# Optimization experiments

Hardware: AMD Instinct MI355X
Metric: run time of the kernel (lower is better)

Reference implementation:

```python
import jax, jax.numpy as jnp
import numpy as np

N_HEAD, D_MODEL, D_HEAD = 16, 1024, 64
QLEN, BSZ, RLEN = 2048, 2, 2048
SCALE = 1.0 / (D_HEAD ** 0.5)


def _rel_shift(x):
    # x: (qlen, rlen, bsz, n_head) -- faithful port of the pad/reshape trick
    q, r, b, n = x.shape
    zero_pad = jnp.zeros((q, 1, b, n), dtype=x.dtype)
    x_padded = jnp.concatenate([zero_pad, x], axis=1)      # (q, r+1, b, n)
    x_padded = x_padded.reshape(r + 1, q, b, n)
    return x_padded[1:].reshape(q, r, b, n)


def setup_inputs() -> dict:
    key = jax.random.key(0)
    ks = jax.random.split(key, 8)
    w = jax.random.normal(ks[0], (QLEN, BSZ, D_MODEL), dtype=jnp.float32)
    r = jax.random.normal(ks[1], (RLEN, D_MODEL), dtype=jnp.float32)
    attn_mask = jax.random.randint(ks[2], (RLEN, BSZ), 0, 2).astype(bool)  # (klen, bsz) key padding
    s = 0.02
    qkv_w = jax.random.normal(ks[3], (D_MODEL, 3 * N_HEAD * D_HEAD), dtype=jnp.float32) * s
    r_net_w = jax.random.normal(ks[4], (D_MODEL, N_HEAD * D_HEAD), dtype=jnp.float32) * s
    o_w = jax.random.normal(ks[5], (N_HEAD * D_HEAD, D_MODEL), dtype=jnp.float32) * s
    r_w_bias = jax.random.normal(ks[6], (N_HEAD, D_HEAD), dtype=jnp.float32) * s
    r_r_bias = jax.random.normal(ks[7], (N_HEAD, D_HEAD), dtype=jnp.float32) * s
    return {"w": w, "r": r, "attn_mask": attn_mask, "qkv_w": qkv_w,
            "r_net_w": r_net_w, "o_w": o_w, "r_w_bias": r_w_bias, "r_r_bias": r_r_bias}


def reference(w, r, attn_mask, qkv_w, r_net_w, o_w, r_w_bias, r_r_bias):
    qlen, bsz, _ = w.shape
    rlen = r.shape[0]
    klen = qlen  # no mems
    heads = w @ qkv_w                                   # (q, b, 3*H)
    wq, wk, wv = jnp.split(heads, 3, axis=-1)
    wq = wq.reshape(qlen, bsz, N_HEAD, D_HEAD)
    wk = wk.reshape(klen, bsz, N_HEAD, D_HEAD)
    wv = wv.reshape(klen, bsz, N_HEAD, D_HEAD)
    r_head_k = (r @ r_net_w).reshape(rlen, N_HEAD, D_HEAD)
    # NOTE: original code sets r_w_bias = self.r_r_bias (bug preserved faithfully)
    rw_head_q = wq + r_r_bias[None, None]               # (q, b, n, d)
    rr_head_q = wq + r_r_bias[None, None]
    AC = jnp.einsum('qbnd,kbnd->bnqk', rw_head_q, wk)
    BD = jnp.einsum('qbnd,rnd->bnqr', rr_head_q, r_head_k)
    BD = jnp.transpose(BD, (2, 3, 0, 1))                # (q, r, b, n)
    BD = _rel_shift(BD)
    BD = jnp.transpose(BD, (2, 3, 0, 1))[:, :, :, :klen]  # (b, n, q, k)
    attn_score = (AC + BD) * SCALE
    # 2D mask broadcast semantics: (klen, bsz) key-padding mask
    attn_score = jnp.where(attn_mask.T[:, None, None, :], -jnp.inf, attn_score)
    attn_prob = jax.nn.softmax(attn_score.astype(jnp.float32), axis=-1)
    attn_prob = jnp.where(jnp.isnan(attn_prob), 0.0, attn_prob).astype(attn_score.dtype)
    coverage = attn_prob
    attn_vec = jnp.einsum('bnqk,kbnd->qbnd', attn_prob, wv)
    attn_vec = attn_vec.reshape(qlen, bsz, N_HEAD * D_HEAD)
    output = attn_vec @ o_w                             # (q, b, d_model)
    return (output, coverage)
```

## Files before the change

### kernel.cpp

```cpp
#include <hip/hip_runtime.h>
#include <hip/hip_bf16.h>


#define QL 2048
#define KL 2048
#define RL 2048
#define BS 2
#define NHD 16
#define DH 64
#define DM 1024

typedef __hip_bfloat16 bf16;
typedef short v8s __attribute__((ext_vector_type(8)));
typedef float v4f __attribute__((ext_vector_type(4)));

__device__ __forceinline__ bf16 f2b(float x) { return __float2bfloat16(x); }
__device__ __forceinline__ short f2s(float x) {
    return __builtin_bit_cast(short, __float2bfloat16(x));
}

template <int EPI>
__global__ __launch_bounds__(256) void gemm64f(
    const float* __restrict__ A, const float* __restrict__ B,
    int M, int N, int K,
    float* __restrict__ C,
    bf16* __restrict__ Qb, bf16* __restrict__ Wk, bf16* __restrict__ Wvt,
    bf16* __restrict__ Rk, const float* __restrict__ rrb)
{
    __shared__ short As[64][40];
    __shared__ short Bs[64][40];
    const int n0 = blockIdx.x * 64, m0 = blockIdx.y * 64;
    const int t = threadIdx.x, w = t >> 6, lane = t & 63;
    const int quad = lane >> 4, lr = lane & 15;

    v4f acc[4] = {};
    for (int k0 = 0; k0 < K; k0 += 32) {
        {
            const int row = t >> 2, cg = (t & 3) << 3;
            const float* ap = A + (size_t)(m0 + row) * K + k0 + cg;
            float4 a0 = *(const float4*)ap;
            float4 a1 = *(const float4*)(ap + 4);
            v8s pk;
            pk[0] = f2s(a0.x); pk[1] = f2s(a0.y); pk[2] = f2s(a0.z); pk[3] = f2s(a0.w);
            pk[4] = f2s(a1.x); pk[5] = f2s(a1.y); pk[6] = f2s(a1.z); pk[7] = f2s(a1.w);
            *(v8s*)&As[row][cg] = pk;
            const int kk = t >> 3, ng = (t & 7) << 3;
            const float* bp = B + (size_t)(k0 + kk) * N + n0 + ng;
            float4 b0 = *(const float4*)bp;
            float4 b1 = *(const float4*)(bp + 4);
            Bs[ng + 0][kk] = f2s(b0.x); Bs[ng + 1][kk] = f2s(b0.y);
            Bs[ng + 2][kk] = f2s(b0.z); Bs[ng + 3][kk] = f2s(b0.w);
            Bs[ng + 4][kk] = f2s(b1.x); Bs[ng + 5][kk] = f2s(b1.y);
            Bs[ng + 6][kk] = f2s(b1.z); Bs[ng + 7][kk] = f2s(b1.w);
        }
        __syncthreads();
        v8s af = *(const v8s*)&As[16 * w + lr][quad * 8];
#pragma unroll
        for (int ct = 0; ct < 4; ++ct) {
            v8s bfm = *(const v8s*)&Bs[ct * 16 + lr][quad * 8];
            acc[ct] = __builtin_amdgcn_mfma_f32_16x16x32_bf16(af, bfm, acc[ct], 0, 0, 0);
        }
        __syncthreads();
    }

#pragma unroll
    for (int ct = 0; ct < 4; ++ct) {
#pragma unroll
        for (int r = 0; r < 4; ++r) {
            const int gm = m0 + 16 * w + quad * 4 + r;
            const int gn = n0 + ct * 16 + lr;
            float v = acc[ct][r];
            if constexpr (EPI == 0) {
                C[(size_t)gm * N + gn] = v;
            } else if constexpr (EPI == 1) {
                const int q = gm >> 1, b = gm & 1;
                const int sec = gn >> 10, idx = gn & 1023;
                const int n = idx >> 6, d = idx & 63;
                const size_t bn = (size_t)(b * NHD + n);
                if (sec == 0) {
                    v += rrb[n * 64 + d];
                    Qb[(bn * QL + q) * DH + d] = f2b(v);
                } else if (sec == 1) {
                    Wk[(bn * KL + q) * DH + d] = f2b(v);
                } else {
                    Wvt[(bn * DH + d) * KL + q] = f2b(v);
                }
            } else {
                const int n = gn >> 6, d = gn & 63;
                Rk[((size_t)n * RL + gm) * DH + d] = f2b(v);
            }
        }
    }
}

__global__ __launch_bounds__(256) void attn_kernel(
    const bf16* __restrict__ Qb, const bf16* __restrict__ Wk,
    const bf16* __restrict__ Wvt, const bf16* __restrict__ Rk,
    const int* __restrict__ mask,
    float* __restrict__ cov, float* __restrict__ AV)
{
    __shared__ short mlds[KL];
    __shared__ short Plds[4][16][32];
    __shared__ float Vbuf[2][4][16][16];
    __shared__ float Lbuf[2][2][16];
    const int bn = blockIdx.y, b = bn >> 4, n = bn & 15;
    const int t = threadIdx.x, w = t >> 6, lane = t & 63;
    const int quad = lane >> 4, lr = lane & 15;
    const int qt = w >> 1, kh = w & 1;
    const int q0 = blockIdx.x * 32 + qt * 16;
    const int kbs = kh * (KL / 2), kbe = kbs + (KL / 2);

    for (int i = t; i < KL; i += 256) mlds[i] = (short)mask[i * BS + b];
    __syncthreads();

    const bf16* qbase = Qb + ((size_t)bn * QL + q0 + lr) * DH;
    const v8s aq0 = *(const v8s*)(qbase + quad * 8);
    const v8s aq1 = *(const v8s*)(qbase + 32 + quad * 8);
    int qs = q0 + 1 + lr; qs = qs > QL - 1 ? QL - 1 : qs;
    const bf16* qsb = Qb + ((size_t)bn * QL + qs) * DH;
    const v8s as0 = *(const v8s*)(qsb + quad * 8);
    const v8s as1 = *(const v8s*)(qsb + 32 + quad * 8);

    const bf16* kbase = Wk + (size_t)bn * KL * DH;
    const bf16* rkb   = Rk + (size_t)n * RL * DH;
    float* covb = cov + (size_t)bn * QL * KL;

    int o_[4], src_[4];
#pragma unroll
    for (int r = 0; r < 4; ++r) {
        const int rho = quad * 4 + r;
        o_[r] = lr - rho;
        src_[r] = (lane & 48) | (o_[r] & 15);
    }

    auto band = [&](int cb, v8s a0, v8s a1) -> v4f {
        int rrow = cb + lr;
        rrow = rrow < 0 ? 0 : (rrow > RL - 1 ? RL - 1 : rrow);
        const bf16* rp = rkb + (size_t)rrow * DH;
        v8s b0 = *(const v8s*)(rp + quad * 8);
        v8s b1 = *(const v8s*)(rp + 32 + quad * 8);
        v4f a = {};
        a = __builtin_amdgcn_mfma_f32_16x16x32_bf16(a0, b0, a, 0, 0, 0);
        a = __builtin_amdgcn_mfma_f32_16x16x32_bf16(a1, b1, a, 0, 0, 0);
        return a;
    };

    auto loadK = [&](int kb, v8s& k0, v8s& k1) {
        const bf16* krow = kbase + (size_t)(kb + lr) * DH;
        k0 = *(const v8s*)(krow + quad * 8);
        k1 = *(const v8s*)(krow + 32 + quad * 8);
    };

    v4f TA0, TA1 = {}, TB0, TB1 = {};

    auto scores = [&](int kb, v8s ck0, v8s ck1, float* e) {
        const bool useA = (kb <= q0);
        const bool useB = (kb >= q0);
        if (useA) TA1 = band(kb - q0 + 2047, aq0, aq1);
        if (useB) TB1 = band(kb - q0 - 2,   as0, as1);
        v4f ac = {};
        ac = __builtin_amdgcn_mfma_f32_16x16x32_bf16(aq0, ck0, ac, 0, 0, 0);
        ac = __builtin_amdgcn_mfma_f32_16x16x32_bf16(aq1, ck1, ac, 0, 0, 0);
        const bool msk = mlds[kb + lr] != 0;
#pragma unroll
        for (int r = 0; r < 4; ++r) {
            const int dk = (kb - q0) + o_[r];
            float vA = 0.f, vB = 0.f;
            if (useA) {
                float x0 = __shfl(TA0[r], src_[r], 64);
                float x1 = __shfl(TA1[r], src_[r], 64);
                vA = (o_[r] >= 0) ? x1 : x0;
            }
            if (useB) {
                float x0 = __shfl(TB0[r], src_[r], 64);
                float x1 = __shfl(TB1[r], src_[r], 64);
                vB = (o_[r] >= 0) ? x1 : x0;
            }
            const float bd = (dk <= 0) ? vA : ((dk == 1) ? 0.f : vB);
            const float ex = __expf((ac[r] + bd) * 0.125f);
            e[r] = msk ? 0.f : ex;
        }
        if (useA) TA0 = TA1;
        if (useB) TB0 = TB1;
    };

    float pl[4] = {0.f, 0.f, 0.f, 0.f};
    TA0 = band(kbs - 16 - q0 + 2047, aq0, aq1);
    TB0 = band(kbs - 16 - q0 - 2,   as0, as1);
    v8s ck0, ck1;
    loadK(kbs, ck0, ck1);
    for (int kb = kbs; kb < kbe; kb += 16) {
        v8s nk0, nk1;
        const int kn = (kb + 16 < KL) ? kb + 16 : kb;
        loadK(kn, nk0, nk1);
        float e[4];
        scores(kb, ck0, ck1, e);
#pragma unroll
        for (int r = 0; r < 4; ++r) pl[r] += e[r];
        ck0 = nk0; ck1 = nk1;
    }
#pragma unroll
    for (int r = 0; r < 4; ++r) {
        float l = pl[r];
#pragma unroll
        for (int off = 1; off < 16; off <<= 1) l += __shfl_xor(l, off, 64);
        pl[r] = l;
    }
    if (lr == 0) {
#pragma unroll
        for (int r = 0; r < 4; ++r) Lbuf[qt][kh][quad * 4 + r] = pl[r];
    }
    __syncthreads();
#pragma unroll
    for (int r = 0; r < 4; ++r) {
        const float lt = Lbuf[qt][0][quad * 4 + r] + Lbuf[qt][1][quad * 4 + r];
        pl[r] = (lt > 0.f) ? 1.f / lt : 0.f;
    }

    v4f accv[4] = {};
    TA0 = band(kbs - 16 - q0 + 2047, aq0, aq1);
    TB0 = band(kbs - 16 - q0 - 2,   as0, as1);
    loadK(kbs, ck0, ck1);
    for (int kb = kbs; kb < kbe; kb += 16) {
        v8s nk0, nk1;
        const int kn = (kb + 16 < KL) ? kb + 16 : kb;
        loadK(kn, nk0, nk1);
        float e[4];
        scores(kb, ck0, ck1, e);
        const int tt = (kb >> 4) & 1;
#pragma unroll
        for (int r = 0; r < 4; ++r) {
            const int q = q0 + quad * 4 + r;
            const float p = e[r] * pl[r];
            covb[(size_t)q * KL + kb + lr] = p;
            Plds[w][quad * 4 + r][tt * 16 + lr] = f2s(p);
        }
        if (tt == 1) {
            v8s ap = *(const v8s*)&Plds[w][lr][quad * 8];
            const int k0 = kb & ~31;
#pragma unroll
            for (int dt = 0; dt < 4; ++dt) {
                const bf16* vrow = Wvt + ((size_t)bn * DH + dt * 16 + lr) * KL + k0 + quad * 8;
                v8s bv = *(const v8s*)vrow;
                accv[dt] = __builtin_amdgcn_mfma_f32_16x16x32_bf16(ap, bv, accv[dt], 0, 0, 0);
            }
        }
        ck0 = nk0; ck1 = nk1;
    }

    if (kh == 1) {
#pragma unroll
        for (int dt = 0; dt < 4; ++dt)
#pragma unroll
            for (int r = 0; r < 4; ++r)
                Vbuf[qt][dt][quad * 4 + r][lr] = accv[dt][r];
    }
    __syncthreads();
    if (kh == 0) {
#pragma unroll
        for (int dt = 0; dt < 4; ++dt) {
#pragma unroll
            for (int r = 0; r < 4; ++r) {
                const int q = q0 + quad * 4 + r;
                const float v = accv[dt][r] + Vbuf[qt][dt][quad * 4 + r][lr];
                AV[((size_t)q * BS + b) * DM + n * DH + dt * 16 + lr] = v;
            }
        }
    }
}

extern "C" void kernel_launch(void* const* d_in, const int* in_sizes, int n_in,
                              void* d_out, int out_size, void* d_ws, size_t ws_size,
                              hipStream_t stream)
{
    const float* w     = (const float*)d_in[0];
    const float* r     = (const float*)d_in[1];
    const int*   mask  = (const int*)d_in[2];
    const float* qkvw  = (const float*)d_in[3];
    const float* rnetw = (const float*)d_in[4];
    const float* ow    = (const float*)d_in[5];
    const float* rrb   = (const float*)d_in[7];

    char* ws = (char*)d_ws;
    bf16*  Qb  = (bf16*)(ws);
    bf16*  Wk  = (bf16*)(ws + ((size_t)8  << 20));
    bf16*  Wvt = (bf16*)(ws + ((size_t)16 << 20));
    bf16*  Rk  = (bf16*)(ws + ((size_t)24 << 20));
    float* AV  = (float*)(ws + ((size_t)28 << 20));

    float* out_main = (float*)d_out;
    float* out_cov  = out_main + (size_t)QL * BS * DM;

    gemm64f<1><<<dim3(48, 64), 256, 0, stream>>>(w, qkvw, 4096, 3072, 1024,
                                                 nullptr, Qb, Wk, Wvt, nullptr, rrb);
    gemm64f<2><<<dim3(16, 32), 256, 0, stream>>>(r, rnetw, 2048, 1024, 1024,
                                                 nullptr, nullptr, nullptr, nullptr, Rk, nullptr);
    attn_kernel<<<dim3(64, 32), 256, 0, stream>>>(Qb, Wk, Wvt, Rk, mask, out_cov, AV);
    gemm64f<0><<<dim3(16, 64), 256, 0, stream>>>(AV, ow, 4096, 1024, 1024,
                                                 out_main, nullptr, nullptr, nullptr, nullptr, nullptr);
}
```

Measured before the change: 1.364 ms.

## Split attention into separate row-sum and output kernels with key-half partials

The single attention kernel is split into two kernels. Pass A computes partial softmax denominators for each key half and writes them to global memory. Pass B recomputes the scores, normalizes them, writes coverage and accumulates P·V into per-half partial buffers, which the output GEMM sums while loading its A operand. This removes in-block LDS reductions and __syncthreads, gives each block four independent query tiles, and adds occupancy hints. In exchange it adds an extra launch, global round trips for the partial sums, and twice the AV read traffic in the final GEMM.

```diff
diff --git a/kernel.cpp b/kernel.cpp
--- a/kernel.cpp
+++ b/kernel.cpp
@@ -21,7 +21,8 @@
 
 template <int EPI>
 __global__ __launch_bounds__(256) void gemm64f(
-    const float* __restrict__ A, const float* __restrict__ B,
+    const float* __restrict__ A, const float* __restrict__ A2,
+    const float* __restrict__ B,
     int M, int N, int K,
     float* __restrict__ C,
     bf16* __restrict__ Qb, bf16* __restrict__ Wk, bf16* __restrict__ Wvt,
@@ -37,9 +38,15 @@
     for (int k0 = 0; k0 < K; k0 += 32) {
         {
             const int row = t >> 2, cg = (t & 3) << 3;
-            const float* ap = A + (size_t)(m0 + row) * K + k0 + cg;
-            float4 a0 = *(const float4*)ap;
-            float4 a1 = *(const float4*)(ap + 4);
+            const size_t aoff = (size_t)(m0 + row) * K + k0 + cg;
+            float4 a0 = *(const float4*)(A + aoff);
+            float4 a1 = *(const float4*)(A + aoff + 4);
+            if (EPI == 0 && A2 != nullptr) {
+                float4 c0 = *(const float4*)(A2 + aoff);
+                float4 c1 = *(const float4*)(A2 + aoff + 4);
+                a0.x += c0.x; a0.y += c0.y; a0.z += c0.z; a0.w += c0.w;
+                a1.x += c1.x; a1.y += c1.y; a1.z += c1.z; a1.w += c1.w;
+            }
             v8s pk;
             pk[0] = f2s(a0.x); pk[1] = f2s(a0.y); pk[2] = f2s(a0.z); pk[3] = f2s(a0.w);
             pk[4] = f2s(a1.x); pk[5] = f2s(a1.y); pk[6] = f2s(a1.z); pk[7] = f2s(a1.w);
@@ -93,24 +100,20 @@
     }
 }
 
-__global__ __launch_bounds__(256) void attn_kernel(
+__global__ __launch_bounds__(256, 8) void attn_passA(
     const bf16* __restrict__ Qb, const bf16* __restrict__ Wk,
-    const bf16* __restrict__ Wvt, const bf16* __restrict__ Rk,
-    const int* __restrict__ mask,
-    float* __restrict__ cov, float* __restrict__ AV)
+    const bf16* __restrict__ Rk, const int* __restrict__ mask,
+    float* __restrict__ lpart)
 {
-    __shared__ short mlds[KL];
-    __shared__ short Plds[4][16][32];
-    __shared__ float Vbuf[2][4][16][16];
-    __shared__ float Lbuf[2][2][16];
+    __shared__ short mlds[KL / 2];
     const int bn = blockIdx.y, b = bn >> 4, n = bn & 15;
+    const int z = blockIdx.z;
     const int t = threadIdx.x, w = t >> 6, lane = t & 63;
     const int quad = lane >> 4, lr = lane & 15;
-    const int qt = w >> 1, kh = w & 1;
-    const int q0 = blockIdx.x * 32 + qt * 16;
-    const int kbs = kh * (KL / 2), kbe = kbs + (KL / 2);
-
-    for (int i = t; i < KL; i += 256) mlds[i] = (short)mask[i * BS + b];
+    const int q0 = blockIdx.x * 64 + w * 16;
+    const int kbs = z * (KL / 2), kbe = kbs + (KL / 2);
+
+    for (int i = t; i < KL / 2; i += 256) mlds[i] = (short)mask[(kbs + i) * BS + b];
     __syncthreads();
 
     const bf16* qbase = Qb + ((size_t)bn * QL + q0 + lr) * DH;
@@ -123,7 +126,6 @@
 
     const bf16* kbase = Wk + (size_t)bn * KL * DH;
     const bf16* rkb   = Rk + (size_t)n * RL * DH;
-    float* covb = cov + (size_t)bn * QL * KL;
 
     int o_[4], src_[4];
 #pragma unroll
@@ -145,23 +147,23 @@
         return a;
     };
 
-    auto loadK = [&](int kb, v8s& k0, v8s& k1) {
-        const bf16* krow = kbase + (size_t)(kb + lr) * DH;
-        k0 = *(const v8s*)(krow + quad * 8);
-        k1 = *(const v8s*)(krow + 32 + quad * 8);
-    };
-
     v4f TA0, TA1 = {}, TB0, TB1 = {};
-
-    auto scores = [&](int kb, v8s ck0, v8s ck1, float* e) {
+    TA0 = band(kbs - 16 - q0 + 2047, aq0, aq1);
+    TB0 = band(kbs - 16 - q0 - 2,   as0, as1);
+
+    float pl[4] = {0.f, 0.f, 0.f, 0.f};
+    for (int kb = kbs; kb < kbe; kb += 16) {
         const bool useA = (kb <= q0);
         const bool useB = (kb >= q0);
         if (useA) TA1 = band(kb - q0 + 2047, aq0, aq1);
         if (useB) TB1 = band(kb - q0 - 2,   as0, as1);
+        const bf16* krow = kbase + (size_t)(kb + lr) * DH;
+        v8s bk0 = *(const v8s*)(krow + quad * 8);
+        v8s bk1 = *(const v8s*)(krow + 32 + quad * 8);
         v4f ac = {};
-        ac = __builtin_amdgcn_mfma_f32_16x16x32_bf16(aq0, ck0, ac, 0, 0, 0);
-        ac = __builtin_amdgcn_mfma_f32_16x16x32_bf16(aq1, ck1, ac, 0, 0, 0);
-        const bool msk = mlds[kb + lr] != 0;
+        ac = __builtin_amdgcn_mfma_f32_16x16x32_bf16(aq0, bk0, ac, 0, 0, 0);
+        ac = __builtin_amdgcn_mfma_f32_16x16x32_bf16(aq1, bk1, ac, 0, 0, 0);
+        const bool msk = mlds[kb - kbs + lr] != 0;
 #pragma unroll
         for (int r = 0; r < 4; ++r) {
             const int dk = (kb - q0) + o_[r];
@@ -178,63 +180,129 @@
             }
             const float bd = (dk <= 0) ? vA : ((dk == 1) ? 0.f : vB);
             const float ex = __expf((ac[r] + bd) * 0.125f);
-            e[r] = msk ? 0.f : ex;
+            pl[r] += msk ? 0.f : ex;
         }
         if (useA) TA0 = TA1;
         if (useB) TB0 = TB1;
+    }
+#pragma unroll
+    for (int r = 0; r < 4; ++r) {
+        float l = pl[r];
+#pragma unroll
+        for (int off = 1; off < 16; off <<= 1) l += __shfl_xor(l, off, 64);
+        pl[r] = l;
+    }
+    if (lr == 0) {
+#pragma unroll
+        for (int r = 0; r < 4; ++r) {
+            const int q = q0 + quad * 4 + r;
+            lpart[((size_t)z * 32 + bn) * QL + q] = pl[r];
+        }
+    }
+}
+
+__global__ __launch_bounds__(256, 6) void attn_passB(
+    const bf16* __restrict__ Qb, const bf16* __restrict__ Wk,
+    const bf16* __restrict__ Wvt, const bf16* __restrict__ Rk,
+    const int* __restrict__ mask, const float* __restrict__ lpart,
+    float* __restrict__ cov, float* __restrict__ AVp0,
+    float* __restrict__ AVp1)
+{
+    __shared__ short mlds[KL / 2];
+    __shared__ short Plds[4][16][32];
+    const int bn = blockIdx.y, b = bn >> 4, n = bn & 15;
+    const int z = blockIdx.z;
+    const int t = threadIdx.x, w = t >> 6, lane = t & 63;
+    const int quad = lane >> 4, lr = lane & 15;
+    const int q0 = blockIdx.x * 64 + w * 16;
+    const int kbs = z * (KL / 2), kbe = kbs + (KL / 2);
+    float* __restrict__ AV = z ? AVp1 : AVp0;
+
+    for (int i = t; i < KL / 2; i += 256) mlds[i] = (short)mask[(kbs + i) * BS + b];
+    __syncthreads();
+
+    float pli[4];
+#pragma unroll
+    for (int r = 0; r < 4; ++r) {
+        const int q = q0 + quad * 4 + r;
+        const float lt = lpart[(size_t)bn * QL + q] +
+                         lpart[((size_t)32 + bn) * QL + q];
+        pli[r] = (lt > 0.f) ? 1.f / lt : 0.f;
+    }
+
+    const bf16* qbase = Qb + ((size_t)bn * QL + q0 + lr) * DH;
+    const v8s aq0 = *(const v8s*)(qbase + quad * 8);
+    const v8s aq1 = *(const v8s*)(qbase + 32 + quad * 8);
+    int qs = q0 + 1 + lr; qs = qs > QL - 1 ? QL - 1 : qs;
+    const bf16* qsb = Qb + ((size_t)bn * QL + qs) * DH;
+    const v8s as0 = *(const v8s*)(qsb + quad * 8);
+    const v8s as1 = *(const v8s*)(qsb + 32 + quad * 8);
+
+    const bf16* kbase = Wk + (size_t)bn * KL * DH;
+    const bf16* rkb   = Rk + (size_t)n * RL * DH;
+    float* covb = cov + (size_t)bn * QL * KL;
+
+    int o_[4], src_[4];
+#pragma unroll
+    for (int r = 0; r < 4; ++r) {
+        const int rho = quad * 4 + r;
+        o_[r] = lr - rho;
+        src_[r] = (lane & 48) | (o_[r] & 15);
+    }
+
+    auto band = [&](int cb, v8s a0, v8s a1) -> v4f {
+        int rrow = cb + lr;
+        rrow = rrow < 0 ? 0 : (rrow > RL - 1 ? RL - 1 : rrow);
+        const bf16* rp = rkb + (size_t)rrow * DH;
+        v8s b0 = *(const v8s*)(rp + quad * 8);
+        v8s b1 = *(const v8s*)(rp + 32 + quad * 8);
+        v4f a = {};
+        a = __builtin_amdgcn_mfma_f32_16x16x32_bf16(a0, b0, a, 0, 0, 0);
+        a = __builtin_amdgcn_mfma_f32_16x16x32_bf16(a1, b1, a, 0, 0, 0);
+        return a;
     };
 
-    float pl[4] = {0.f, 0.f, 0.f, 0.f};
+    v4f TA0, TA1 = {}, TB0, TB1 = {};
     TA0 = band(kbs - 16 - q0 + 2047, aq0, aq1);
     TB0 = band(kbs - 16 - q0 - 2,   as0, as1);
-    v8s ck0, ck1;
-    loadK(kbs, ck0, ck1);
+
+    v4f accv[4] = {};
     for (int kb = kbs; kb < kbe; kb += 16) {
-        v8s nk0, nk1;
-        const int kn = (kb + 16 < KL) ? kb + 16 : kb;
-        loadK(kn, nk0, nk1);
-        float e[4];
-        scores(kb, ck0, ck1, e);
-#pragma unroll
-        for (int r = 0; r < 4; ++r) pl[r] += e[r];
-        ck0 = nk0; ck1 = nk1;
-    }
-#pragma unroll
-    for (int r = 0; r < 4; ++r) {
-        float l = pl[r];
-#pragma unroll
-        for (int off = 1; off < 16; off <<= 1) l += __shfl_xor(l, off, 64);
-        pl[r] = l;
-    }
-    if (lr == 0) {
-#pragma unroll
-        for (int r = 0; r < 4; ++r) Lbuf[qt][kh][quad * 4 + r] = pl[r];
-    }
-    __syncthreads();
-#pragma unroll
-    for (int r = 0; r < 4; ++r) {
-        const float lt = Lbuf[qt][0][quad * 4 + r] + Lbuf[qt][1][quad * 4 + r];
-        pl[r] = (lt > 0.f) ? 1.f / lt : 0.f;
-    }
-
-    v4f accv[4] = {};
-    TA0 = band(kbs - 16 - q0 + 2047, aq0, aq1);
-    TB0 = band(kbs - 16 - q0 - 2,   as0, as1);
-    loadK(kbs, ck0, ck1);
-    for (int kb = kbs; kb < kbe; kb += 16) {
-        v8s nk0, nk1;
-        const int kn = (kb + 16 < KL) ? kb + 16 : kb;
-        loadK(kn, nk0, nk1);
-        float e[4];
-        scores(kb, ck0, ck1, e);
+        const bool useA = (kb <= q0);
+        const bool useB = (kb >= q0);
+        if (useA) TA1 = band(kb - q0 + 2047, aq0, aq1);
+        if (useB) TB1 = band(kb - q0 - 2,   as0, as1);
+        const bf16* krow = kbase + (size_t)(kb + lr) * DH;
+        v8s bk0 = *(const v8s*)(krow + quad * 8);
+        v8s bk1 = *(const v8s*)(krow + 32 + quad * 8);
+        v4f ac = {};
+        ac = __builtin_amdgcn_mfma_f32_16x16x32_bf16(aq0, bk0, ac, 0, 0, 0);
+        ac = __builtin_amdgcn_mfma_f32_16x16x32_bf16(aq1, bk1, ac, 0, 0, 0);
+        const bool msk = mlds[kb - kbs + lr] != 0;
         const int tt = (kb >> 4) & 1;
 #pragma unroll
         for (int r = 0; r < 4; ++r) {
+            const int dk = (kb - q0) + o_[r];
+            float vA = 0.f, vB = 0.f;
+            if (useA) {
+                float x0 = __shfl(TA0[r], src_[r], 64);
+                float x1 = __shfl(TA1[r], src_[r], 64);
+                vA = (o_[r] >= 0) ? x1 : x0;
+            }
+            if (useB) {
+                float x0 = __shfl(TB0[r], src_[r], 64);
+                float x1 = __shfl(TB1[r], src_[r], 64);
+                vB = (o_[r] >= 0) ? x1 : x0;
+            }
+            const float bd = (dk <= 0) ? vA : ((dk == 1) ? 0.f : vB);
+            const float ex = __expf((ac[r] + bd) * 0.125f);
+            const float p = (msk ? 0.f : ex) * pli[r];
             const int q = q0 + quad * 4 + r;
-            const float p = e[r] * pl[r];
             covb[(size_t)q * KL + kb + lr] = p;
             Plds[w][quad * 4 + r][tt * 16 + lr] = f2s(p);
         }
+        if (useA) TA0 = TA1;
+        if (useB) TB0 = TB1;
         if (tt == 1) {
             v8s ap = *(const v8s*)&Plds[w][lr][quad * 8];
             const int k0 = kb & ~31;
@@ -245,26 +313,14 @@
                 accv[dt] = __builtin_amdgcn_mfma_f32_16x16x32_bf16(ap, bv, accv[dt], 0, 0, 0);
             }
         }
-        ck0 = nk0; ck1 = nk1;
-    }
-
-    if (kh == 1) {
-#pragma unroll
-        for (int dt = 0; dt < 4; ++dt)
-#pragma unroll
-            for (int r = 0; r < 4; ++r)
-                Vbuf[qt][dt][quad * 4 + r][lr] = accv[dt][r];
-    }
-    __syncthreads();
-    if (kh == 0) {
-#pragma unroll
-        for (int dt = 0; dt < 4; ++dt) {
-#pragma unroll
-            for (int r = 0; r < 4; ++r) {
-                const int q = q0 + quad * 4 + r;
-                const float v = accv[dt][r] + Vbuf[qt][dt][quad * 4 + r][lr];
-                AV[((size_t)q * BS + b) * DM + n * DH + dt * 16 + lr] = v;
-            }
+    }
+
+#pragma unroll
+    for (int dt = 0; dt < 4; ++dt) {
+#pragma unroll
+        for (int r = 0; r < 4; ++r) {
+            const int q = q0 + quad * 4 + r;
+            AV[((size_t)q * BS + b) * DM + n * DH + dt * 16 + lr] = accv[dt][r];
         }
     }
 }
@@ -282,20 +338,24 @@
     const float* rrb   = (const float*)d_in[7];
 
     char* ws = (char*)d_ws;
-    bf16*  Qb  = (bf16*)(ws);
-    bf16*  Wk  = (bf16*)(ws + ((size_t)8  << 20));
-    bf16*  Wvt = (bf16*)(ws + ((size_t)16 << 20));
-    bf16*  Rk  = (bf16*)(ws + ((size_t)24 << 20));
-    float* AV  = (float*)(ws + ((size_t)28 << 20));
+    bf16*  Qb   = (bf16*)(ws);
+    bf16*  Wk   = (bf16*)(ws + ((size_t)8  << 20));
+    bf16*  Wvt  = (bf16*)(ws + ((size_t)16 << 20));
+    bf16*  Rk   = (bf16*)(ws + ((size_t)24 << 20));
+    float* AVp0 = (float*)(ws + ((size_t)28 << 20));
+    float* AVp1 = (float*)(ws + ((size_t)44 << 20));
+    float* lpart = (float*)(ws + ((size_t)60 << 20));
 
     float* out_main = (float*)d_out;
     float* out_cov  = out_main + (size_t)QL * BS * DM;
 
-    gemm64f<1><<<dim3(48, 64), 256, 0, stream>>>(w, qkvw, 4096, 3072, 1024,
+    gemm64f<1><<<dim3(48, 64), 256, 0, stream>>>(w, nullptr, qkvw, 4096, 3072, 1024,
                                                  nullptr, Qb, Wk, Wvt, nullptr, rrb);
-    gemm64f<2><<<dim3(16, 32), 256, 0, stream>>>(r, rnetw, 2048, 1024, 1024,
+    gemm64f<2><<<dim3(16, 32), 256, 0, stream>>>(r, nullptr, rnetw, 2048, 1024, 1024,
                                                  nullptr, nullptr, nullptr, nullptr, Rk, nullptr);
-    attn_kernel<<<dim3(64, 32), 256, 0, stream>>>(Qb, Wk, Wvt, Rk, mask, out_cov, AV);
-    gemm64f<0><<<dim3(16, 64), 256, 0, stream>>>(AV, ow, 4096, 1024, 1024,
+    attn_passA<<<dim3(32, 32, 2), 256, 0, stream>>>(Qb, Wk, Rk, mask, lpart);
+    attn_passB<<<dim3(32, 32, 2), 256, 0, stream>>>(Qb, Wk, Wvt, Rk, mask, lpart,
+                                                    out_cov, AVp0, AVp1);
+    gemm64f<0><<<dim3(16, 64), 256, 0, stream>>>(AVp0, AVp1, ow, 4096, 1024, 1024,
                                                  out_main, nullptr, nullptr, nullptr, nullptr, nullptr);
 }
```

After: 1.749 ms. 28.3% more time.
